# Kernel optimization log

Hardware: AMD Instinct MI355X
Metric: run time of the kernel (lower is better)

## Reference

```python
import jax, jax.numpy as jnp
import numpy as np

LEAK = 0.2

def _leaky(h):
    return jnp.where(h >= 0, h, LEAK * h)

def setup_inputs() -> dict:
    key = jax.random.key(0)
    ks = jax.random.split(key, 12)
    B, C, H, W = 4, 19, 256, 512
    ndf = 64
    dims = [C, ndf, ndf * 2, ndf * 4, ndf * 8, 1]  # 19->64->128->256->512->1
    inp = {
        "x": jax.random.normal(ks[0], (B, C, H, W), dtype=jnp.float32),
        "lbl": jax.random.uniform(ks[1], (B, H, W), dtype=jnp.float32),
    }
    for i in range(5):
        fan_in = dims[i]
        scale = 1.0 / np.sqrt(fan_in)
        inp[f"W{i+1}"] = jax.random.uniform(ks[2 + 2 * i], (dims[i + 1], dims[i]), minval=-scale, maxval=scale, dtype=jnp.float32)
        inp[f"b{i+1}"] = jax.random.uniform(ks[3 + 2 * i], (dims[i + 1],), minval=-scale, maxval=scale, dtype=jnp.float32)
    return inp

def reference(x, lbl, W1, b1, W2, b2, W3, b3, W4, b4, W5, b5):
    # x: [B, C, H, W] -> [B, H, W, C]; 1x1 convs == per-pixel linear layers
    h = jnp.transpose(x, (0, 2, 3, 1))
    h = _leaky(jnp.einsum('bhwc,oc->bhwo', h, W1) + b1)
    h = _leaky(jnp.einsum('bhwc,oc->bhwo', h, W2) + b2)
    h = _leaky(jnp.einsum('bhwc,oc->bhwo', h, W3) + b3)
    h = _leaky(jnp.einsum('bhwc,oc->bhwo', h, W4) + b4)
    z = (jnp.einsum('bhwc,oc->bhwo', h, W5) + b5)[..., 0]  # logits [B,H,W]
    # stable BCE-with-logits, mean over all elements; equals the per-pixel
    # mean-over-batch losses summed and divided by H*W as in the original loop
    bce = jnp.maximum(z, 0.0) - z * lbl + jnp.log1p(jnp.exp(-jnp.abs(z)))
    return jnp.mean(bce)
```

## Files before the change

kernel.cpp:

```cpp
#include <hip/hip_runtime.h>


#define HW_ 131072
#define NPIX 524288

using bf16x8 = __attribute__((ext_vector_type(8))) short;
using f32x4  = __attribute__((ext_vector_type(4))) float;

#define MFMA __builtin_amdgcn_mfma_f32_16x16x32_bf16
#define PRIO1 __builtin_amdgcn_s_setprio(1)
#define PRIO0 __builtin_amdgcn_s_setprio(0)

__device__ __forceinline__ unsigned short f2bf(float f) {
  unsigned u = __builtin_bit_cast(unsigned, f);
  u += 0x7FFFu + ((u >> 16) & 1u);
  return (unsigned short)(u >> 16);
}

__device__ __forceinline__ int kinv(int k) {
  return ((k >> 5) << 5) + (((k >> 2) & 1) << 4) + (((k >> 3) & 3) << 2) + (k & 3);
}

#define OW1 0
#define OW2 2048
#define OW3 10240
#define OW4 43008
#define WTOT 174080

template <int K0, int KP, bool PERM>
__device__ __forceinline__ void conv_layer(const float* __restrict__ W,
                                           unsigned short* __restrict__ out,
                                           int i) {
  int r9 = i & 511;
  int lane = r9 >> 3, j = r9 & 7;
  int frag = i >> 9;
  constexpr int KS = KP / 32;
  int ob = frag / KS, ks = frag - ob * KS;
  int o = ob * 16 + (lane & 15);
  int k = ks * 32 + ((lane >> 4) << 3) + j;
  int f = PERM ? kinv(k) : k;
  out[i] = f2bf(f < K0 ? W[o * K0 + f] : 0.f);
}

__global__ void wconv_kernel(const float* __restrict__ W1, const float* __restrict__ W2,
                             const float* __restrict__ W3, const float* __restrict__ W4,
                             unsigned short* __restrict__ wb) {
  int i = blockIdx.x * 256 + threadIdx.x;
  if (i < OW2) {
    conv_layer<19, 32, false>(W1, wb + OW1, i - OW1);
  } else if (i < OW3) {
    conv_layer<64, 64, true>(W2, wb + OW2, i - OW2);
  } else if (i < OW4) {
    conv_layer<128, 128, true>(W3, wb + OW3, i - OW3);
  } else if (i < WTOT) {
    conv_layer<256, 256, true>(W4, wb + OW4, i - OW4);
  }
}

__device__ __forceinline__ f32x4 leaky4(f32x4 v) {
  f32x4 r;
#pragma unroll
  for (int i = 0; i < 4; i++) r[i] = fmaxf(v[i], 0.2f * v[i]);
  return r;
}

__device__ __forceinline__ unsigned cvtpk(float lo, float hi) {
  unsigned r;
  asm("v_cvt_pk_bf16_f32 %0, %1, %2" : "=v"(r) : "v"(lo), "v"(hi));
  return r;
}
__device__ __forceinline__ bf16x8 pack8(f32x4 e, f32x4 o) {
  union { unsigned u[4]; bf16x8 v; } r;
  r.u[0] = cvtpk(e[0], e[1]);
  r.u[1] = cvtpk(e[2], e[3]);
  r.u[2] = cvtpk(o[0], o[1]);
  r.u[3] = cvtpk(o[2], o[3]);
  return r.v;
}

__device__ __forceinline__ void gl16(const unsigned char* g, unsigned char* l) {
  __builtin_amdgcn_global_load_lds(
      (const __attribute__((address_space(1))) unsigned int*)(const void*)g,
      (__attribute__((address_space(3))) unsigned int*)(void*)l, 16, 0, 0);
}
__device__ __forceinline__ void stage_n(const unsigned char* __restrict__ g,
                                        unsigned char* l, int nseg,
                                        int wave, int lane) {
  for (int s = wave; s < nseg; s += 4)
    gl16(g + (s << 10) + (lane << 4), l + (s << 10));
}

#define LDF(bufp, lf) (*(const bf16x8*)((bufp) + ((lf) << 10) + (lane << 4)))

__global__ __launch_bounds__(256) __attribute__((amdgpu_waves_per_eu(3, 3)))
void disc_lds(const float* __restrict__ x, const float* __restrict__ lbl,
              const unsigned short* __restrict__ wb,
              const float* __restrict__ b1, const float* __restrict__ b2,
              const float* __restrict__ b3, const float* __restrict__ b4,
              const float* __restrict__ W5f, const float* __restrict__ b5,
              float* __restrict__ out) {
  __shared__ __align__(16) unsigned char sb0[24576];
  __shared__ __align__(16) unsigned char sb1[24576];

  int t = threadIdx.x;
  int wave = t >> 6, lane = t & 63;
  int g = lane >> 4, li = lane & 15;
  long px0 = ((long)blockIdx.x * 4 + wave) * 32;
  int b = (int)(px0 >> 17);
  int hw0 = (int)(px0 & (HW_ - 1));
  const unsigned char* wb8 = (const unsigned char*)wb;

  stage_n(wb8, sb0, 20, wave, lane);
  __syncthreads();

  stage_n(wb8 + 20480, sb1, 24, wave, lane);

  bf16x8 xb[2];
#pragma unroll
  for (int pb = 0; pb < 2; pb++) {
    const float* xp = x + (((long)b * 19) << 17) + hw0 + pb * 16 + li;
    bf16x8 v;
#pragma unroll
    for (int j = 0; j < 8; j++) {
      int c = 8 * g + j;
      float f = (c < 19) ? xp[(long)c << 17] : 0.f;
      v[j] = (short)f2bf(f);
    }
    xb[pb] = v;
  }

  bf16x8 h1[2][2];
#pragma unroll
  for (int obp = 0; obp < 2; obp++) {
    bf16x8 fE = LDF(sb0, 2 * obp);
    bf16x8 fO = LDF(sb0, 2 * obp + 1);
    f32x4 bE = *(const f32x4*)(b1 + 32 * obp + 4 * g);
    f32x4 bO = *(const f32x4*)(b1 + 32 * obp + 16 + 4 * g);
    f32x4 aE[2], aO[2];
    PRIO1;
#pragma unroll
    for (int pb = 0; pb < 2; pb++) {
      aE[pb] = MFMA(fE, xb[pb], bE, 0, 0, 0);
      aO[pb] = MFMA(fO, xb[pb], bO, 0, 0, 0);
    }
    PRIO0;
#pragma unroll
    for (int pb = 0; pb < 2; pb++)
      h1[pb][obp] = pack8(leaky4(aE[pb]), leaky4(aO[pb]));
  }

  bf16x8 h2[2][4];
#pragma unroll
  for (int obp = 0; obp < 4; obp++) {
    bf16x8 fE0 = LDF(sb0, 4 + 4 * obp);
    bf16x8 fE1 = LDF(sb0, 4 + 4 * obp + 1);
    bf16x8 fO0 = LDF(sb0, 4 + 4 * obp + 2);
    bf16x8 fO1 = LDF(sb0, 4 + 4 * obp + 3);
    f32x4 bE = *(const f32x4*)(b2 + 32 * obp + 4 * g);
    f32x4 bO = *(const f32x4*)(b2 + 32 * obp + 16 + 4 * g);
    f32x4 aE[2], aO[2];
    PRIO1;
#pragma unroll
    for (int pb = 0; pb < 2; pb++) {
      aE[pb] = MFMA(fE0, h1[pb][0], bE, 0, 0, 0);
      aE[pb] = MFMA(fE1, h1[pb][1], aE[pb], 0, 0, 0);
      aO[pb] = MFMA(fO0, h1[pb][0], bO, 0, 0, 0);
      aO[pb] = MFMA(fO1, h1[pb][1], aO[pb], 0, 0, 0);
    }
    PRIO0;
#pragma unroll
    for (int pb = 0; pb < 2; pb++)
      h2[pb][obp] = pack8(leaky4(aE[pb]), leaky4(aO[pb]));
  }
  __syncthreads();

  bf16x8 h3[2][8];
  stage_n(wb8 + 45056, sb0, 24, wave, lane);
#pragma unroll
  for (int ol = 0; ol < 3; ol++) {
    int obp = ol;
    int lfE = ol * 8, lfO = ol * 8 + 4;
    f32x4 bE = *(const f32x4*)(b3 + 32 * obp + 4 * g);
    f32x4 bO = *(const f32x4*)(b3 + 32 * obp + 16 + 4 * g);
    f32x4 aE[2], aO[2];
#pragma unroll
    for (int pb = 0; pb < 2; pb++) { aE[pb] = bE; aO[pb] = bO; }
    PRIO1;
#pragma unroll
    for (int ks = 0; ks < 4; ks++) {
      bf16x8 fE = LDF(sb1, lfE + ks);
      bf16x8 fO = LDF(sb1, lfO + ks);
#pragma unroll
      for (int pb = 0; pb < 2; pb++) {
        aE[pb] = MFMA(fE, h2[pb][ks], aE[pb], 0, 0, 0);
        aO[pb] = MFMA(fO, h2[pb][ks], aO[pb], 0, 0, 0);
      }
    }
    PRIO0;
#pragma unroll
    for (int pb = 0; pb < 2; pb++)
      h3[pb][obp] = pack8(leaky4(aE[pb]), leaky4(aO[pb]));
  }
  __syncthreads();

  stage_n(wb8 + 69632, sb1, 16, wave, lane);
#pragma unroll
  for (int ol = 0; ol < 3; ol++) {
    int obp = 3 + ol;
    int lfE = ol * 8, lfO = ol * 8 + 4;
    f32x4 bE = *(const f32x4*)(b3 + 32 * obp + 4 * g);
    f32x4 bO = *(const f32x4*)(b3 + 32 * obp + 16 + 4 * g);
    f32x4 aE[2], aO[2];
#pragma unroll
    for (int pb = 0; pb < 2; pb++) { aE[pb] = bE; aO[pb] = bO; }
    PRIO1;
#pragma unroll
    for (int ks = 0; ks < 4; ks++) {
      bf16x8 fE = LDF(sb0, lfE + ks);
      bf16x8 fO = LDF(sb0, lfO + ks);
#pragma unroll
      for (int pb = 0; pb < 2; pb++) {
        aE[pb] = MFMA(fE, h2[pb][ks], aE[pb], 0, 0, 0);
        aO[pb] = MFMA(fO, h2[pb][ks], aO[pb], 0, 0, 0);
      }
    }
    PRIO0;
#pragma unroll
    for (int pb = 0; pb < 2; pb++)
      h3[pb][obp] = pack8(leaky4(aE[pb]), leaky4(aO[pb]));
  }
  __syncthreads();

  stage_n(wb8 + 86016, sb0, 24, wave, lane);
#pragma unroll
  for (int ol = 0; ol < 2; ol++) {
    int obp = 6 + ol;
    int lfE = ol * 8, lfO = ol * 8 + 4;
    f32x4 bE = *(const f32x4*)(b3 + 32 * obp + 4 * g);
    f32x4 bO = *(const f32x4*)(b3 + 32 * obp + 16 + 4 * g);
    f32x4 aE[2], aO[2];
#pragma unroll
    for (int pb = 0; pb < 2; pb++) { aE[pb] = bE; aO[pb] = bO; }
    PRIO1;
#pragma unroll
    for (int ks = 0; ks < 4; ks++) {
      bf16x8 fE = LDF(sb1, lfE + ks);
      bf16x8 fO = LDF(sb1, lfO + ks);
#pragma unroll
      for (int pb = 0; pb < 2; pb++) {
        aE[pb] = MFMA(fE, h2[pb][ks], aE[pb], 0, 0, 0);
        aO[pb] = MFMA(fO, h2[pb][ks], aO[pb], 0, 0, 0);
      }
    }
    PRIO0;
#pragma unroll
    for (int pb = 0; pb < 2; pb++)
      h3[pb][obp] = pack8(leaky4(aE[pb]), leaky4(aO[pb]));
  }
  __syncthreads();

  f32x4 zp[2];
#pragma unroll
  for (int pb = 0; pb < 2; pb++) zp[pb] = f32x4{0.f, 0.f, 0.f, 0.f};

#pragma unroll 1
  for (int j = 0; j < 11; j++) {
    const unsigned char* cur = (j & 1) ? sb1 : sb0;
    unsigned char* nxt = (j & 1) ? sb0 : sb1;
    if (j < 10) {
      int nseg = (j < 9) ? 24 : 16;
      stage_n(wb8 + 86016 + (j + 1) * 24576, nxt, nseg, wave, lane);
    }
    int nobs = (j < 10) ? 3 : 2;
    for (int oo = 0; oo < nobs; oo++) {
      int ob = 3 * j + oo;
      f32x4 bv = *(const f32x4*)(b4 + 16 * ob + 4 * g);
      f32x4 w5v = *(const f32x4*)(W5f + 16 * ob + 4 * g);
      f32x4 a[2];
#pragma unroll
      for (int pb = 0; pb < 2; pb++) a[pb] = bv;
      PRIO1;
#pragma unroll
      for (int ks = 0; ks < 8; ks++) {
        bf16x8 f4 = LDF(cur, oo * 8 + ks);
#pragma unroll
        for (int pb = 0; pb < 2; pb++) a[pb] = MFMA(f4, h3[pb][ks], a[pb], 0, 0, 0);
      }
      PRIO0;
#pragma unroll
      for (int pb = 0; pb < 2; pb++) {
        f32x4 lv = leaky4(a[pb]);
#pragma unroll
        for (int i = 0; i < 4; i++) zp[pb][i] = fmaf(lv[i], w5v[i], zp[pb][i]);
      }
    }
    __syncthreads();
  }

  float zb[2];
#pragma unroll
  for (int pb = 0; pb < 2; pb++) {
    float s = zp[pb][0] + zp[pb][1] + zp[pb][2] + zp[pb][3];
    s += __shfl_xor(s, 16);
    s += __shfl_xor(s, 32);
    zb[pb] = s;
  }
  float w = 0.f;
  if (lane < 32) {
    float z = ((lane & 16) ? zb[1] : zb[0]) + b5[0];
    float lab = lbl[px0 + lane];
    w = fmaxf(z, 0.f) - z * lab + log1pf(expf(-fabsf(z)));
  }
#pragma unroll
  for (int m = 1; m <= 32; m <<= 1) w += __shfl_xor(w, m);
  float* zsp = (float*)sb0;
  if (lane == 0) zsp[wave] = w;
  __syncthreads();
  if (t == 0)
    atomicAdd(out, (zsp[0] + zsp[1] + zsp[2] + zsp[3]) * (1.f / (float)NPIX));
}

#define LDAG(dst, Wf, K0, KP, PERM, ob, ks)                                    \
  do {                                                                         \
    int o_ = (ob) * 16 + li;                                                   \
    for (int j_ = 0; j_ < 8; j_++) {                                           \
      int k_ = (ks) * 32 + (g << 3) + j_;                                      \
      int f_ = (PERM) ? kinv(k_) : k_;                                         \
      float v_ = f_ < (K0) ? (Wf)[o_ * (K0) + f_] : 0.f;                       \
      dst[j_] = (short)f2bf(v_);                                               \
    }                                                                          \
  } while (0)

__global__ __launch_bounds__(256, 1) void disc_fb(
    const float* __restrict__ x, const float* __restrict__ lbl,
    const float* __restrict__ W1f, const float* __restrict__ b1,
    const float* __restrict__ W2f, const float* __restrict__ b2,
    const float* __restrict__ W3f, const float* __restrict__ b3,
    const float* __restrict__ W4f, const float* __restrict__ b4,
    const float* __restrict__ W5f, const float* __restrict__ b5,
    float* __restrict__ out) {
  __shared__ float zs[4];
  int t = threadIdx.x;
  int wave = t >> 6, lane = t & 63;
  int g = lane >> 4, li = lane & 15;
  long px0 = ((long)blockIdx.x * 4 + wave) * 64;
  int b = (int)(px0 >> 17);
  int hw0 = (int)(px0 & (HW_ - 1));

  bf16x8 xb[4];
#pragma unroll
  for (int pb = 0; pb < 4; pb++) {
    const float* xp = x + (((long)b * 19) << 17) + hw0 + pb * 16 + li;
    bf16x8 v;
#pragma unroll
    for (int j = 0; j < 8; j++) {
      int c = 8 * g + j;
      float f = (c < 19) ? xp[(long)c << 17] : 0.f;
      v[j] = (short)f2bf(f);
    }
    xb[pb] = v;
  }

  bf16x8 h1[4][2];
#pragma unroll
  for (int obp = 0; obp < 2; obp++) {
    bf16x8 fE, fO;
    LDAG(fE, W1f, 19, 32, false, 2 * obp, 0);
    LDAG(fO, W1f, 19, 32, false, 2 * obp + 1, 0);
    f32x4 bE = *(const f32x4*)(b1 + 32 * obp + 4 * g);
    f32x4 bO = *(const f32x4*)(b1 + 32 * obp + 16 + 4 * g);
#pragma unroll
    for (int pb = 0; pb < 4; pb++) {
      f32x4 aE = MFMA(fE, xb[pb], bE, 0, 0, 0);
      f32x4 aO = MFMA(fO, xb[pb], bO, 0, 0, 0);
      h1[pb][obp] = pack8(leaky4(aE), leaky4(aO));
    }
  }

  bf16x8 h2[4][4];
#pragma unroll
  for (int obp = 0; obp < 4; obp++) {
    bf16x8 fE0, fE1, fO0, fO1;
    LDAG(fE0, W2f, 64, 64, true, 2 * obp, 0);
    LDAG(fE1, W2f, 64, 64, true, 2 * obp, 1);
    LDAG(fO0, W2f, 64, 64, true, 2 * obp + 1, 0);
    LDAG(fO1, W2f, 64, 64, true, 2 * obp + 1, 1);
    f32x4 bE = *(const f32x4*)(b2 + 32 * obp + 4 * g);
    f32x4 bO = *(const f32x4*)(b2 + 32 * obp + 16 + 4 * g);
#pragma unroll
    for (int pb = 0; pb < 4; pb++) {
      f32x4 aE = MFMA(fE0, h1[pb][0], bE, 0, 0, 0);
      aE = MFMA(fE1, h1[pb][1], aE, 0, 0, 0);
      f32x4 aO = MFMA(fO0, h1[pb][0], bO, 0, 0, 0);
      aO = MFMA(fO1, h1[pb][1], aO, 0, 0, 0);
      h2[pb][obp] = pack8(leaky4(aE), leaky4(aO));
    }
  }

  bf16x8 h3[4][8];
#pragma unroll
  for (int obp = 0; obp < 8; obp++) {
    f32x4 bE = *(const f32x4*)(b3 + 32 * obp + 4 * g);
    f32x4 bO = *(const f32x4*)(b3 + 32 * obp + 16 + 4 * g);
    f32x4 aE[4], aO[4];
#pragma unroll
    for (int pb = 0; pb < 4; pb++) { aE[pb] = bE; aO[pb] = bO; }
#pragma unroll
    for (int ks = 0; ks < 4; ks++) {
      bf16x8 fE, fO;
      LDAG(fE, W3f, 128, 128, true, 2 * obp, ks);
      LDAG(fO, W3f, 128, 128, true, 2 * obp + 1, ks);
#pragma unroll
      for (int pb = 0; pb < 4; pb++) {
        aE[pb] = MFMA(fE, h2[pb][ks], aE[pb], 0, 0, 0);
        aO[pb] = MFMA(fO, h2[pb][ks], aO[pb], 0, 0, 0);
      }
    }
#pragma unroll
    for (int pb = 0; pb < 4; pb++)
      h3[pb][obp] = pack8(leaky4(aE[pb]), leaky4(aO[pb]));
  }

  f32x4 zp[4];
#pragma unroll
  for (int pb = 0; pb < 4; pb++) zp[pb] = f32x4{0.f, 0.f, 0.f, 0.f};

  for (int ob = 0; ob < 32; ob++) {
    f32x4 bv = *(const f32x4*)(b4 + 16 * ob + 4 * g);
    f32x4 w5v = *(const f32x4*)(W5f + 16 * ob + 4 * g);
    f32x4 a[4];
#pragma unroll
    for (int pb = 0; pb < 4; pb++) a[pb] = bv;
#pragma unroll
    for (int ks = 0; ks < 8; ks++) {
      bf16x8 f4;
      LDAG(f4, W4f, 256, 256, true, ob, ks);
#pragma unroll
      for (int pb = 0; pb < 4; pb++) a[pb] = MFMA(f4, h3[pb][ks], a[pb], 0, 0, 0);
    }
#pragma unroll
    for (int pb = 0; pb < 4; pb++) {
      f32x4 lv = leaky4(a[pb]);
#pragma unroll
      for (int i = 0; i < 4; i++) zp[pb][i] = fmaf(lv[i], w5v[i], zp[pb][i]);
    }
  }

  float zb[4];
#pragma unroll
  for (int pb = 0; pb < 4; pb++) {
    float s = zp[pb][0] + zp[pb][1] + zp[pb][2] + zp[pb][3];
    s += __shfl_xor(s, 16);
    s += __shfl_xor(s, 32);
    zb[pb] = s;
  }
  float zsel = (g == 0) ? zb[0] : (g == 1) ? zb[1] : (g == 2) ? zb[2] : zb[3];
  float z = zsel + b5[0];
  float lab = lbl[px0 + lane];
  float w = fmaxf(z, 0.f) - z * lab + log1pf(expf(-fabsf(z)));
#pragma unroll
  for (int m = 1; m <= 32; m <<= 1) w += __shfl_xor(w, m);
  if (lane == 0) zs[wave] = w;
  __syncthreads();
  if (t == 0)
    atomicAdd(out, (zs[0] + zs[1] + zs[2] + zs[3]) * (1.f / (float)NPIX));
}

extern "C" void kernel_launch(void* const* d_in, const int* in_sizes, int n_in,
                              void* d_out, int out_size, void* d_ws, size_t ws_size,
                              hipStream_t stream) {
  const float* x   = (const float*)d_in[0];
  const float* lbl = (const float*)d_in[1];
  const float* W1  = (const float*)d_in[2];
  const float* b1  = (const float*)d_in[3];
  const float* W2  = (const float*)d_in[4];
  const float* b2  = (const float*)d_in[5];
  const float* W3  = (const float*)d_in[6];
  const float* b3  = (const float*)d_in[7];
  const float* W4  = (const float*)d_in[8];
  const float* b4  = (const float*)d_in[9];
  const float* W5  = (const float*)d_in[10];
  const float* b5  = (const float*)d_in[11];
  float* out = (float*)d_out;

  hipMemsetAsync(d_out, 0, sizeof(float), stream);

  bool pre = ws_size >= (size_t)WTOT * sizeof(unsigned short);
  if (pre) {
    unsigned short* wbp = (unsigned short*)d_ws;
    wconv_kernel<<<(WTOT + 255) / 256, 256, 0, stream>>>(W1, W2, W3, W4, wbp);
    disc_lds<<<NPIX / 128, 256, 0, stream>>>(x, lbl, wbp, b1, b2, b3, b4, W5, b5, out);
  } else {
    disc_fb<<<NPIX / 256, 256, 0, stream>>>(x, lbl, W1, b1, W2, b2, W3, b3, W4, b4,
                                            W5, b5, out);
  }
}
```

Measured before the change: 192.8 us.

## Drop setprio, rotate layer-4 chunk order per block, unroll obs, use packed FP32 ops

Removes the s_setprio wrappers around the MFMA sections. Each block now starts its layer-4 weight chunk sequence at blockIdx mod 11, so concurrent blocks read different weight chunks instead of all hitting the same one. The inner output-block loop is unrolled into a pair plus an optional third block, which exposes more independent MFMAs. The leaky ReLU and W5 accumulation now use v_pk_mul_f32 and v_pk_fma_f32 inline asm. The rotation changes the floating-point summation order of z, and the inline asm may restrict the compiler's scheduling.

```diff
diff --git a/kernel.cpp b/kernel.cpp
--- a/kernel.cpp
+++ b/kernel.cpp
@@ -6,10 +6,9 @@
 
 using bf16x8 = __attribute__((ext_vector_type(8))) short;
 using f32x4  = __attribute__((ext_vector_type(4))) float;
+using f32x2  = __attribute__((ext_vector_type(2))) float;
 
 #define MFMA __builtin_amdgcn_mfma_f32_16x16x32_bf16
-#define PRIO1 __builtin_amdgcn_s_setprio(1)
-#define PRIO0 __builtin_amdgcn_s_setprio(0)
 
 __device__ __forceinline__ unsigned short f2bf(float f) {
   unsigned u = __builtin_bit_cast(unsigned, f);
@@ -57,10 +56,26 @@
   }
 }
 
+__device__ __forceinline__ f32x2 pk_mul(f32x2 a, f32x2 b) {
+  f32x2 d;
+  asm("v_pk_mul_f32 %0, %1, %2" : "=v"(d) : "v"(a), "v"(b));
+  return d;
+}
+__device__ __forceinline__ f32x2 pk_fma(f32x2 a, f32x2 b, f32x2 c) {
+  f32x2 d;
+  asm("v_pk_fma_f32 %0, %1, %2, %3" : "=v"(d) : "v"(a), "v"(b), "v"(c));
+  return d;
+}
+
 __device__ __forceinline__ f32x4 leaky4(f32x4 v) {
+  f32x2 c = {0.2f, 0.2f};
+  f32x2 lo = {v[0], v[1]}, hi = {v[2], v[3]};
+  f32x2 ml = pk_mul(lo, c), mh = pk_mul(hi, c);
   f32x4 r;
-#pragma unroll
-  for (int i = 0; i < 4; i++) r[i] = fmaxf(v[i], 0.2f * v[i]);
+  r[0] = fmaxf(v[0], ml[0]);
+  r[1] = fmaxf(v[1], ml[1]);
+  r[2] = fmaxf(v[2], mh[0]);
+  r[3] = fmaxf(v[3], mh[1]);
   return r;
 }
 
@@ -137,13 +152,11 @@
     f32x4 bE = *(const f32x4*)(b1 + 32 * obp + 4 * g);
     f32x4 bO = *(const f32x4*)(b1 + 32 * obp + 16 + 4 * g);
     f32x4 aE[2], aO[2];
-    PRIO1;
 #pragma unroll
     for (int pb = 0; pb < 2; pb++) {
       aE[pb] = MFMA(fE, xb[pb], bE, 0, 0, 0);
       aO[pb] = MFMA(fO, xb[pb], bO, 0, 0, 0);
     }
-    PRIO0;
 #pragma unroll
     for (int pb = 0; pb < 2; pb++)
       h1[pb][obp] = pack8(leaky4(aE[pb]), leaky4(aO[pb]));
@@ -159,7 +172,6 @@
     f32x4 bE = *(const f32x4*)(b2 + 32 * obp + 4 * g);
     f32x4 bO = *(const f32x4*)(b2 + 32 * obp + 16 + 4 * g);
     f32x4 aE[2], aO[2];
-    PRIO1;
 #pragma unroll
     for (int pb = 0; pb < 2; pb++) {
       aE[pb] = MFMA(fE0, h1[pb][0], bE, 0, 0, 0);
@@ -167,7 +179,6 @@
       aO[pb] = MFMA(fO0, h1[pb][0], bO, 0, 0, 0);
       aO[pb] = MFMA(fO1, h1[pb][1], aO[pb], 0, 0, 0);
     }
-    PRIO0;
 #pragma unroll
     for (int pb = 0; pb < 2; pb++)
       h2[pb][obp] = pack8(leaky4(aE[pb]), leaky4(aO[pb]));
@@ -185,7 +196,6 @@
     f32x4 aE[2], aO[2];
 #pragma unroll
     for (int pb = 0; pb < 2; pb++) { aE[pb] = bE; aO[pb] = bO; }
-    PRIO1;
 #pragma unroll
     for (int ks = 0; ks < 4; ks++) {
       bf16x8 fE = LDF(sb1, lfE + ks);
@@ -196,7 +206,6 @@
         aO[pb] = MFMA(fO, h2[pb][ks], aO[pb], 0, 0, 0);
       }
     }
-    PRIO0;
 #pragma unroll
     for (int pb = 0; pb < 2; pb++)
       h3[pb][obp] = pack8(leaky4(aE[pb]), leaky4(aO[pb]));
@@ -213,7 +222,6 @@
     f32x4 aE[2], aO[2];
 #pragma unroll
     for (int pb = 0; pb < 2; pb++) { aE[pb] = bE; aO[pb] = bO; }
-    PRIO1;
 #pragma unroll
     for (int ks = 0; ks < 4; ks++) {
       bf16x8 fE = LDF(sb0, lfE + ks);
@@ -224,14 +232,14 @@
         aO[pb] = MFMA(fO, h2[pb][ks], aO[pb], 0, 0, 0);
       }
     }
-    PRIO0;
 #pragma unroll
     for (int pb = 0; pb < 2; pb++)
       h3[pb][obp] = pack8(leaky4(aE[pb]), leaky4(aO[pb]));
   }
   __syncthreads();
 
-  stage_n(wb8 + 86016, sb0, 24, wave, lane);
+  int jc0 = (int)(blockIdx.x % 11u);
+  stage_n(wb8 + 86016 + jc0 * 24576, sb0, (jc0 == 10) ? 16 : 24, wave, lane);
 #pragma unroll
   for (int ol = 0; ol < 2; ol++) {
     int obp = 6 + ol;
@@ -241,7 +249,6 @@
     f32x4 aE[2], aO[2];
 #pragma unroll
     for (int pb = 0; pb < 2; pb++) { aE[pb] = bE; aO[pb] = bO; }
-    PRIO1;
 #pragma unroll
     for (int ks = 0; ks < 4; ks++) {
       bf16x8 fE = LDF(sb1, lfE + ks);
@@ -252,7 +259,6 @@
         aO[pb] = MFMA(fO, h2[pb][ks], aO[pb], 0, 0, 0);
       }
     }
-    PRIO0;
 #pragma unroll
     for (int pb = 0; pb < 2; pb++)
       h3[pb][obp] = pack8(leaky4(aE[pb]), leaky4(aO[pb]));
@@ -267,31 +273,64 @@
   for (int j = 0; j < 11; j++) {
     const unsigned char* cur = (j & 1) ? sb1 : sb0;
     unsigned char* nxt = (j & 1) ? sb0 : sb1;
+    int jc = jc0 + j; if (jc >= 11) jc -= 11;
     if (j < 10) {
-      int nseg = (j < 9) ? 24 : 16;
-      stage_n(wb8 + 86016 + (j + 1) * 24576, nxt, nseg, wave, lane);
-    }
-    int nobs = (j < 10) ? 3 : 2;
-    for (int oo = 0; oo < nobs; oo++) {
-      int ob = 3 * j + oo;
-      f32x4 bv = *(const f32x4*)(b4 + 16 * ob + 4 * g);
-      f32x4 w5v = *(const f32x4*)(W5f + 16 * ob + 4 * g);
-      f32x4 a[2];
-#pragma unroll
-      for (int pb = 0; pb < 2; pb++) a[pb] = bv;
-      PRIO1;
+      int jn = jc + 1 == 11 ? 0 : jc + 1;
+      stage_n(wb8 + 86016 + jn * 24576, nxt, (jn == 10) ? 16 : 24, wave, lane);
+    }
+    int ob0 = 3 * jc;
+    f32x4 bv0 = *(const f32x4*)(b4 + 16 * ob0 + 4 * g);
+    f32x4 bv1 = *(const f32x4*)(b4 + 16 * (ob0 + 1) + 4 * g);
+    f32x4 w50 = *(const f32x4*)(W5f + 16 * ob0 + 4 * g);
+    f32x4 w51 = *(const f32x4*)(W5f + 16 * (ob0 + 1) + 4 * g);
+    {
+      f32x4 a0[2], a1[2];
+#pragma unroll
+      for (int pb = 0; pb < 2; pb++) { a0[pb] = bv0; a1[pb] = bv1; }
 #pragma unroll
       for (int ks = 0; ks < 8; ks++) {
-        bf16x8 f4 = LDF(cur, oo * 8 + ks);
-#pragma unroll
-        for (int pb = 0; pb < 2; pb++) a[pb] = MFMA(f4, h3[pb][ks], a[pb], 0, 0, 0);
-      }
-      PRIO0;
+        bf16x8 f40 = LDF(cur, 0 * 8 + ks);
+        bf16x8 f41 = LDF(cur, 1 * 8 + ks);
+#pragma unroll
+        for (int pb = 0; pb < 2; pb++) {
+          a0[pb] = MFMA(f40, h3[pb][ks], a0[pb], 0, 0, 0);
+          a1[pb] = MFMA(f41, h3[pb][ks], a1[pb], 0, 0, 0);
+        }
+      }
 #pragma unroll
       for (int pb = 0; pb < 2; pb++) {
-        f32x4 lv = leaky4(a[pb]);
-#pragma unroll
-        for (int i = 0; i < 4; i++) zp[pb][i] = fmaf(lv[i], w5v[i], zp[pb][i]);
+        f32x4 l0 = leaky4(a0[pb]), l1 = leaky4(a1[pb]);
+        f32x2 zlo = {zp[pb][0], zp[pb][1]}, zhi = {zp[pb][2], zp[pb][3]};
+        zlo = pk_fma(f32x2{l0[0], l0[1]}, f32x2{w50[0], w50[1]}, zlo);
+        zhi = pk_fma(f32x2{l0[2], l0[3]}, f32x2{w50[2], w50[3]}, zhi);
+        zlo = pk_fma(f32x2{l1[0], l1[1]}, f32x2{w51[0], w51[1]}, zlo);
+        zhi = pk_fma(f32x2{l1[2], l1[3]}, f32x2{w51[2], w51[3]}, zhi);
+        zp[pb][0] = zlo[0]; zp[pb][1] = zlo[1];
+        zp[pb][2] = zhi[0]; zp[pb][3] = zhi[1];
+      }
+    }
+    if (jc != 10) {
+      int ob2 = ob0 + 2;
+      f32x4 bv2 = *(const f32x4*)(b4 + 16 * ob2 + 4 * g);
+      f32x4 w52 = *(const f32x4*)(W5f + 16 * ob2 + 4 * g);
+      f32x4 a2[2];
+#pragma unroll
+      for (int pb = 0; pb < 2; pb++) a2[pb] = bv2;
+#pragma unroll
+      for (int ks = 0; ks < 8; ks++) {
+        bf16x8 f42 = LDF(cur, 2 * 8 + ks);
+#pragma unroll
+        for (int pb = 0; pb < 2; pb++)
+          a2[pb] = MFMA(f42, h3[pb][ks], a2[pb], 0, 0, 0);
+      }
+#pragma unroll
+      for (int pb = 0; pb < 2; pb++) {
+        f32x4 l2 = leaky4(a2[pb]);
+        f32x2 zlo = {zp[pb][0], zp[pb][1]}, zhi = {zp[pb][2], zp[pb][3]};
+        zlo = pk_fma(f32x2{l2[0], l2[1]}, f32x2{w52[0], w52[1]}, zlo);
+        zhi = pk_fma(f32x2{l2[2], l2[3]}, f32x2{w52[2], w52[3]}, zhi);
+        zp[pb][0] = zlo[0]; zp[pb][1] = zlo[1];
+        zp[pb][2] = zhi[0]; zp[pb][3] = zhi[1];
       }
     }
     __syncthreads();
```

Result: slower. 202.9 us (+5.2%).
